# Optimization experiments

Measured on AMD Instinct MI355X. Metric: run time of the kernel, lower is better.

Reference implementation:

```python
import jax, jax.numpy as jnp
import numpy as np

N, F, D, M, B, K = 100000, 256, 128, 10, 32768, 32


def setup_inputs() -> dict:
    key = jax.random.key(0)
    ks = jax.random.split(key, 14)
    stdv = float(1.0 / np.sqrt(D))
    inp = {
        "feature": jax.random.normal(ks[0], (N, F), jnp.float32),
        "flow_char_adj": jax.random.uniform(ks[1], (M, N), jnp.float32),
        "history": jax.random.randint(ks[2], (B, K), 0, N),
        "item_id": jax.random.randint(ks[3], (B,), 0, N),
        "category_r": jax.random.randint(ks[4], (B,), 0, 2),
        "category_n": jax.random.randint(ks[5], (B,), 0, 2),
        "PA_level": jax.random.randint(ks[6], (B,), 0, M),
        # learned parameters (uniform(-stdv, stdv) as in reset_parameters)
        "weight_emb": jax.random.uniform(ks[7], (F, D), jnp.float32, -stdv, stdv),
        "bias_emb": jax.random.uniform(ks[8], (D,), jnp.float32, -stdv, stdv),
        "weight_character": jax.random.uniform(ks[9], (2 * D, D), jnp.float32, -stdv, stdv),
        "att1_w": jax.random.uniform(ks[10], (D, 1), jnp.float32, -stdv, stdv),
        "att1_b": jax.random.uniform(ks[11], (1,), jnp.float32, -stdv, stdv),
        "linear1_w": jax.random.uniform(ks[12], (2 * D, D), jnp.float32, -stdv, stdv),
        "linear1_b": jax.random.uniform(ks[13], (D,), jnp.float32, -stdv, stdv),
    }
    return inp


def reference(feature, flow_char_adj, weight_emb, bias_emb, weight_character,
              att1_w, att1_b, linear1_w, linear1_b,
              history, item_id, category_r, category_n, PA_level):
    # embedding_encode
    flow_emb = feature @ weight_emb + bias_emb              # [N, D]
    character_emb = flow_char_adj @ flow_emb                # [M, D] (spmm)

    # character_modeling (shared for r and n)
    def char_lat(cat, pa):
        ce = jnp.concatenate([character_emb[cat], character_emb[pa]], axis=1)  # [B, 2D]
        return jax.nn.sigmoid(ce @ weight_character)        # [B, D]

    lat_r = char_lat(category_r, PA_level)
    lat_n = char_lat(category_n, PA_level)

    # attribute_agg: mix flow emb with its 2 category embeddings
    flow_all = (flow_emb + flow_char_adj[:2].T @ character_emb[:2]) * 0.5  # [N, D]

    # Flow_Aggregator: per-node neighbor attention (batched over ragged lists,
    # here padded to fixed degree K)
    neigh = flow_all[history]                                # [B, K, D]
    scores = neigh @ att1_w + att1_b                         # [B, K, 1]
    att = jax.nn.softmax(scores, axis=1)                     # softmax over neighbors
    agg = jnp.sum(att * neigh, axis=1)                       # [B, D]

    # NOTE: in the torch source, self_flow_latent is mutated in-place so
    # self_feats aliases neigh_feats -> both halves of the concat equal agg.
    combined = jnp.concatenate([agg, agg], axis=1)           # [B, 2D]
    out = jax.nn.relu(combined @ linear1_w + linear1_b)      # [B, D] (dropout p=0)

    pred_r = jnp.sum(lat_r * out, axis=1)                    # [B]
    pred_n = jnp.sum(lat_n * out, axis=1)                    # [B]
    return pred_r, pred_n
```

## Files before the change

### kernel.cpp

```cpp
#include <hip/hip_runtime.h>
#include <cmath>

#define NN 100000
#define FF 256
#define DDIM 128
#define MM 10
#define BB 32768
#define KK 32
#define NB1 1563
#define NREP 64

#define OFF_Q     0
#define OFF_CEREP 100096
#define OFF_CE    182016
#define OFF_LAT   183296
#define OFF_CE01  185856
#define OFF_CS    186112
#define OFF_AGGB  186128
#define OFF_FE8   2283280
#define OFF_WF    5483280
#define OFF_WPF   5499664

typedef __attribute__((ext_vector_type(8))) short bf16x8;
typedef __attribute__((ext_vector_type(4))) float floatx4;
typedef __attribute__((ext_vector_type(2))) float floatx2;

__device__ __forceinline__ unsigned short f2bf(float x) {
  union { float f; unsigned u; } v; v.f = x;
  unsigned r = v.u + 0x7FFFu + ((v.u >> 16) & 1u);
  return (unsigned short)(r >> 16);
}

__device__ __forceinline__ bf16x8 cvt8(float4 a, float4 b) {
  short h[8];
  h[0] = (short)f2bf(a.x); h[1] = (short)f2bf(a.y);
  h[2] = (short)f2bf(a.z); h[3] = (short)f2bf(a.w);
  h[4] = (short)f2bf(b.x); h[5] = (short)f2bf(b.y);
  h[6] = (short)f2bf(b.z); h[7] = (short)f2bf(b.w);
  return *reinterpret_cast<bf16x8*>(h);
}

__global__ __launch_bounds__(256) void k0_wprep(const float* __restrict__ wemb,
                                                const float* __restrict__ l1w,
                                                short* __restrict__ wf,
                                                short* __restrict__ wpf)
{
  const int t = blockIdx.x * 256 + threadIdx.x;
  if (t < 4096) {
    const int kk = t >> 9, rem = t & 511;
    const int ct = rem >> 6, l = rem & 63;
    const int n = ct * 16 + (l & 15);
    const int kbase = kk * 32 + (l >> 4) * 8;
    short hi[8];
#pragma unroll
    for (int j = 0; j < 8; j++) hi[j] = (short)f2bf(wemb[(kbase + j) * 128 + n]);
    *reinterpret_cast<int4*>(&wf[((kk * 8 + ct) * 64 + l) * 8]) = *reinterpret_cast<int4*>(hi);
  } else {
    const int t2 = t - 4096;
    const int kk = t2 >> 9, rem = t2 & 511;
    const int ct = rem >> 6, l = rem & 63;
    const int n = ct * 16 + (l & 15);
    short h[8];
#pragma unroll
    for (int j = 0; j < 8; j++) {
      const int kp = kk * 32 + (l >> 4) * 8 + j;
      const int i = ((kp & 7) << 4) | (kp >> 3);
      h[j] = (short)f2bf(l1w[i * 128 + n] + l1w[(128 + i) * 128 + n]);
    }
    *reinterpret_cast<int4*>(&wpf[((kk * 8 + ct) * 64 + l) * 8]) = *reinterpret_cast<int4*>(h);
  }
}

__global__ __launch_bounds__(256) void k1_fused(const float* __restrict__ feat,
    const short* __restrict__ wf, const float* __restrict__ bemb,
    const float* __restrict__ attw, const float* __restrict__ adj,
    float* __restrict__ q, unsigned char* __restrict__ fe8,
    float* __restrict__ cerep)
{
  __shared__ __align__(16) unsigned char ldst[128 * 144];
  const int tid = threadIdx.x;
  const int wv = tid >> 6, l = tid & 63;
  const int lane16 = l & 15, quad = l >> 4;
  const int rowbase = blockIdx.x * 64 + wv * 16;

  floatx4 acc[8];
#pragma unroll
  for (int ct = 0; ct < 8; ct++) acc[ct] = floatx4{0.f, 0.f, 0.f, 0.f};

  int r0 = rowbase + lane16; if (r0 > NN - 1) r0 = NN - 1;
  const float* pa = &feat[(size_t)r0 * 256 + quad * 8];

  float4 A[4][2];
#pragma unroll
  for (int i = 0; i < 4; i++) {
    A[i][0] = *reinterpret_cast<const float4*>(pa + i * 32);
    A[i][1] = *reinterpret_cast<const float4*>(pa + i * 32 + 4);
  }
#pragma unroll
  for (int kk = 0; kk < 8; kk++) {
    const bf16x8 a0 = cvt8(A[kk & 3][0], A[kk & 3][1]);
    if (kk < 4) {
      A[kk & 3][0] = *reinterpret_cast<const float4*>(pa + (kk + 4) * 32);
      A[kk & 3][1] = *reinterpret_cast<const float4*>(pa + (kk + 4) * 32 + 4);
    }
    const short* wb = &wf[kk * 4096 + l * 8];
#pragma unroll
    for (int ct = 0; ct < 8; ct++) {
      const bf16x8 bh = *reinterpret_cast<const bf16x8*>(&wb[ct * 512]);
      acc[ct] = __builtin_amdgcn_mfma_f32_16x16x32_bf16(a0, bh, acc[ct], 0, 0, 0);
    }
  }

  float bembv[8], attwv[8];
#pragma unroll
  for (int ct = 0; ct < 8; ct++) {
    bembv[ct] = bemb[ct * 16 + lane16];
    attwv[ct] = attw[ct * 16 + lane16];
  }
#pragma unroll
  for (int reg = 0; reg < 4; reg++) {
    const int r = rowbase + quad * 4 + reg;
    float v[8]; float qp = 0.f;
#pragma unroll
    for (int ct = 0; ct < 8; ct++) {
      v[ct] = acc[ct][reg] + bembv[ct];
      qp = fmaf(v[ct], attwv[ct], qp);
    }
    acc[0][reg] = v[0]; acc[1][reg] = v[1]; acc[2][reg] = v[2]; acc[3][reg] = v[3];
    acc[4][reg] = v[4]; acc[5][reg] = v[5]; acc[6][reg] = v[6]; acc[7][reg] = v[7];
    qp += __shfl_xor(qp, 1, 16);
    qp += __shfl_xor(qp, 2, 16);
    qp += __shfl_xor(qp, 4, 16);
    qp += __shfl_xor(qp, 8, 16);
    if (r < NN) {
      unsigned u0 = __builtin_amdgcn_cvt_pk_fp8_f32(v[0], v[1], 0, false);
      u0 = __builtin_amdgcn_cvt_pk_fp8_f32(v[2], v[3], u0, true);
      unsigned u1 = __builtin_amdgcn_cvt_pk_fp8_f32(v[4], v[5], 0, false);
      u1 = __builtin_amdgcn_cvt_pk_fp8_f32(v[6], v[7], u1, true);
      *reinterpret_cast<uint2*>(&fe8[(size_t)r * 128 + lane16 * 8]) = make_uint2(u0, u1);
      if (lane16 == 0) q[r] = 0.5f * qp;
    }
  }
#pragma unroll
  for (int rp = 0; rp < 2; rp++) {
    const int rloc = wv * 16 + quad * 4 + rp * 2;
    const int g0 = blockIdx.x * 64 + rloc;
#pragma unroll
    for (int ct = 0; ct < 8; ct++) {
      const unsigned short h0 = (g0     < NN) ? f2bf(acc[ct][rp * 2])     : (unsigned short)0;
      const unsigned short h1 = (g0 + 1 < NN) ? f2bf(acc[ct][rp * 2 + 1]) : (unsigned short)0;
      const unsigned pk = (unsigned)h0 | ((unsigned)h1 << 16);
      *reinterpret_cast<unsigned*>(&ldst[(ct * 16 + lane16) * 144 + rloc * 2]) = pk;
    }
  }
  __syncthreads();

  floatx4 cacc[2];
  cacc[0] = floatx4{0.f, 0.f, 0.f, 0.f};
  cacc[1] = floatx4{0.f, 0.f, 0.f, 0.f};
  const int mclamp = (lane16 < 10) ? lane16 : 9;
#pragma unroll
  for (int kc = 0; kc < 2; kc++) {
    int n0 = blockIdx.x * 64 + kc * 32 + quad * 8;
    if (n0 > NN - 8) n0 = NN - 8;
    const float4 f0 = *reinterpret_cast<const float4*>(&adj[(size_t)mclamp * NN + n0]);
    const float4 f1 = *reinterpret_cast<const float4*>(&adj[(size_t)mclamp * NN + n0 + 4]);
    const bf16x8 afr = cvt8(f0, f1);
#pragma unroll
    for (int tt = 0; tt < 2; tt++) {
      const int col = (wv * 2 + tt) * 16 + lane16;
      const bf16x8 bfr = *reinterpret_cast<const bf16x8*>(
          &ldst[col * 144 + (kc * 32 + quad * 8) * 2]);
      cacc[tt] = __builtin_amdgcn_mfma_f32_16x16x32_bf16(afr, bfr, cacc[tt], 0, 0, 0);
    }
  }
  float* myrep = &cerep[(blockIdx.x & (NREP - 1)) * 1280];
#pragma unroll
  for (int tt = 0; tt < 2; tt++) {
#pragma unroll
    for (int reg = 0; reg < 4; reg++) {
      const int m = quad * 4 + reg;
      if (m < 10)
        atomicAdd(&myrep[m * 128 + (wv * 2 + tt) * 16 + lane16], cacc[tt][reg]);
    }
  }
}

__global__ __launch_bounds__(256) void k3r_reduce(const float* __restrict__ cerep,
                                                  float* __restrict__ ce)
{
  const int o = blockIdx.x * 256 + threadIdx.x;
  if (o < 1280) {
    float s = 0.f;
#pragma unroll 8
    for (int r = 0; r < NREP; r++) s += cerep[r * 1280 + o];
    ce[o] = s;
  }
}

__global__ __launch_bounds__(128) void k3_prep(const float* __restrict__ ce,
    const float* __restrict__ wchar, const float* __restrict__ attw,
    float* __restrict__ latTab, float* __restrict__ ce01p, float* __restrict__ cs)
{
  const int blk = blockIdx.x, tid = threadIdx.x;
  __shared__ float cec[128], cep[128];
  if (blk < 20) {
    const int c = blk / 10, p = blk % 10;
    cec[tid] = ce[c * 128 + tid];
    cep[tid] = ce[p * 128 + tid];
    __syncthreads();
    float s = 0.f;
#pragma unroll 4
    for (int j = 0; j < 128; j++) {
      s = fmaf(cec[j], wchar[j * 128 + tid], s);
      s = fmaf(cep[j], wchar[(128 + j) * 128 + tid], s);
    }
    latTab[blk * 128 + tid] = 1.f / (1.f + expf(-s));
  } else {
    const float s0 = ce[tid];
    const float s1 = ce[128 + tid];
    const int pidx = (tid & 15) * 8 + (tid >> 4);
    ce01p[pidx] = s0;
    ce01p[128 + pidx] = s1;
    cec[tid] = s0 * attw[tid];
    cep[tid] = s1 * attw[tid];
    __syncthreads();
    if (tid < 64) {
      float p0 = cec[tid] + cec[tid + 64];
      float p1 = cep[tid] + cep[tid + 64];
#pragma unroll
      for (int off = 32; off >= 1; off >>= 1) {
        p0 += __shfl_xor(p0, off);
        p1 += __shfl_xor(p1, off);
      }
      if (tid == 0) { cs[0] = 0.5f * p0; cs[1] = 0.5f * p1; }
    }
  }
}

__global__ __launch_bounds__(256) void k4a_attn(const unsigned char* __restrict__ fe8,
    const float* __restrict__ q, const float* __restrict__ adj,
    const int* __restrict__ history, const float* __restrict__ cs,
    const float* __restrict__ attb_p, const float* __restrict__ ce01p,
    short* __restrict__ aggb)
{
  const int tid = threadIdx.x;
  const int lane = tid & 63;
  const int wv = tid >> 6;
  const int half = lane >> 5;
  const int t = lane & 31;
  const int b = blockIdx.x * 8 + wv * 2 + half;

  const int n_my = history[b * 32 + t];
  const float a0 = adj[n_my];
  const float a1 = adj[NN + n_my];
  const float sc = q[n_my] + a0 * cs[0] + a1 * cs[1] + attb_p[0];
  float m = sc;
#pragma unroll
  for (int off = 16; off >= 1; off >>= 1) m = fmaxf(m, __shfl_xor(m, off, 32));
  const float e = expf(sc - m);
  float sum = e;
#pragma unroll
  for (int off = 16; off >= 1; off >>= 1) sum += __shfl_xor(sum, off, 32);
  const float att = e / sum;
  float p0 = att * a0, p1 = att * a1;
#pragma unroll
  for (int off = 16; off >= 1; off >>= 1) {
    p0 += __shfl_xor(p0, off, 32);
    p1 += __shfl_xor(p1, off, 32);
  }

  float4 acc = make_float4(0.f, 0.f, 0.f, 0.f);
#pragma unroll
  for (int k = 0; k < 32; k++) {
    const int nk = __shfl(n_my, k, 32);
    const float ak = __shfl(att, k, 32);
    const unsigned u = *reinterpret_cast<const unsigned*>(&fe8[(size_t)nk * 128 + t * 4]);
    const floatx2 lo = __builtin_amdgcn_cvt_pk_f32_fp8(u, false);
    const floatx2 hi = __builtin_amdgcn_cvt_pk_f32_fp8(u, true);
    acc.x = fmaf(ak, lo[0], acc.x);
    acc.y = fmaf(ak, lo[1], acc.y);
    acc.z = fmaf(ak, hi[0], acc.z);
    acc.w = fmaf(ak, hi[1], acc.w);
  }
  const int col = t * 4;
  const float4 c0 = *reinterpret_cast<const float4*>(&ce01p[col]);
  const float4 c1 = *reinterpret_cast<const float4*>(&ce01p[128 + col]);
  const float ox = 0.5f * (acc.x + p0 * c0.x + p1 * c1.x);
  const float oy = 0.5f * (acc.y + p0 * c0.y + p1 * c1.y);
  const float oz = 0.5f * (acc.z + p0 * c0.z + p1 * c1.z);
  const float ow = 0.5f * (acc.w + p0 * c0.w + p1 * c1.w);
  const unsigned lo_ = (unsigned)f2bf(ox) | ((unsigned)f2bf(oy) << 16);
  const unsigned hi_ = (unsigned)f2bf(oz) | ((unsigned)f2bf(ow) << 16);
  *reinterpret_cast<uint2*>(&aggb[(size_t)b * 128 + col]) = make_uint2(lo_, hi_);
}

__global__ __launch_bounds__(256) void k4b_mfma(const short* __restrict__ aggb,
    const short* __restrict__ wpf, const float* __restrict__ l1b,
    const float* __restrict__ latTab,
    const int* __restrict__ cr, const int* __restrict__ cn, const int* __restrict__ pa,
    float* __restrict__ out)
{
  const int tid = threadIdx.x;
  const int wv = tid >> 6, l = tid & 63;
  const int lane16 = l & 15, quad = l >> 4;
  const int rowbase = blockIdx.x * 128 + wv * 32;
  const int r0 = rowbase + lane16;
  const int r1 = r0 + 16;

  floatx4 acc[2][8];
#pragma unroll
  for (int rt = 0; rt < 2; rt++)
#pragma unroll
    for (int ct = 0; ct < 8; ct++) acc[rt][ct] = floatx4{0.f, 0.f, 0.f, 0.f};

#pragma unroll
  for (int kk = 0; kk < 4; kk++) {
    const bf16x8 a0 = *reinterpret_cast<const bf16x8*>(&aggb[(size_t)r0 * 128 + kk * 32 + quad * 8]);
    const bf16x8 a1 = *reinterpret_cast<const bf16x8*>(&aggb[(size_t)r1 * 128 + kk * 32 + quad * 8]);
    const short* wb = &wpf[kk * 4096 + l * 8];
#pragma unroll
    for (int ct = 0; ct < 8; ct++) {
      const bf16x8 bh = *reinterpret_cast<const bf16x8*>(&wb[ct * 512]);
      acc[0][ct] = __builtin_amdgcn_mfma_f32_16x16x32_bf16(a0, bh, acc[0][ct], 0, 0, 0);
      acc[1][ct] = __builtin_amdgcn_mfma_f32_16x16x32_bf16(a1, bh, acc[1][ct], 0, 0, 0);
    }
  }

  float bb[8];
#pragma unroll
  for (int ct = 0; ct < 8; ct++) bb[ct] = l1b[ct * 16 + lane16];
#pragma unroll
  for (int rt = 0; rt < 2; rt++) {
#pragma unroll
    for (int reg = 0; reg < 4; reg++) {
      const int r = rowbase + rt * 16 + quad * 4 + reg;
      const int ir  = (cr[r] * 10 + pa[r]) * 128;
      const int in_ = (cn[r] * 10 + pa[r]) * 128;
      float pr = 0.f, pn = 0.f;
#pragma unroll
      for (int ct = 0; ct < 8; ct++) {
        const float v = fmaxf(acc[rt][ct][reg] + bb[ct], 0.f);
        pr = fmaf(v, latTab[ir  + ct * 16 + lane16], pr);
        pn = fmaf(v, latTab[in_ + ct * 16 + lane16], pn);
      }
      pr += __shfl_xor(pr, 1, 16); pr += __shfl_xor(pr, 2, 16);
      pr += __shfl_xor(pr, 4, 16); pr += __shfl_xor(pr, 8, 16);
      pn += __shfl_xor(pn, 1, 16); pn += __shfl_xor(pn, 2, 16);
      pn += __shfl_xor(pn, 4, 16); pn += __shfl_xor(pn, 8, 16);
      if (lane16 == 0) { out[r] = pr; out[BB + r] = pn; }
    }
  }
}

extern "C" void kernel_launch(void* const* d_in, const int* in_sizes, int n_in,
                              void* d_out, int out_size, void* d_ws, size_t ws_size,
                              hipStream_t stream) {
  const float* feat  = (const float*)d_in[0];
  const float* adj   = (const float*)d_in[1];
  const int*   hist  = (const int*)d_in[2];
  const int*   cr    = (const int*)d_in[4];
  const int*   cn    = (const int*)d_in[5];
  const int*   pa    = (const int*)d_in[6];
  const float* wemb  = (const float*)d_in[7];
  const float* bemb  = (const float*)d_in[8];
  const float* wchar = (const float*)d_in[9];
  const float* attw  = (const float*)d_in[10];
  const float* attb  = (const float*)d_in[11];
  const float* l1w   = (const float*)d_in[12];
  const float* l1b   = (const float*)d_in[13];
  float* out = (float*)d_out;
  float* ws  = (float*)d_ws;

  float* q     = ws + OFF_Q;
  float* cerep = ws + OFF_CEREP;
  float* ce    = ws + OFF_CE;
  float* lat   = ws + OFF_LAT;
  float* ce01p = ws + OFF_CE01;
  float* cs    = ws + OFF_CS;
  short* aggb  = (short*)(ws + OFF_AGGB);
  unsigned char* fe8 = (unsigned char*)(ws + OFF_FE8);
  short* wf    = (short*)(ws + OFF_WF);
  short* wpf   = (short*)(ws + OFF_WPF);

  hipMemsetAsync(cerep, 0, NREP * 1280 * sizeof(float), stream);
  k0_wprep<<<24, 256, 0, stream>>>(wemb, l1w, wf, wpf);
  k1_fused<<<NB1, 256, 0, stream>>>(feat, wf, bemb, attw, adj, q, fe8, cerep);
  k3r_reduce<<<5, 256, 0, stream>>>(cerep, ce);
  k3_prep<<<21, 128, 0, stream>>>(ce, wchar, attw, lat, ce01p, cs);
  k4a_attn<<<4096, 256, 0, stream>>>(fe8, q, adj, hist, cs, attb, ce01p, aggb);
  k4b_mfma<<<256, 256, 0, stream>>>(aggb, wpf, l1b, lat, cr, cn, pa, out);
}
```

Measured before the change: 268.7 us.

## Retile k1 so each wave computes four row tiles reusing weight fragments

The fused embedding GEMM kernel now uses 128-thread blocks where each wave computes 64 rows (four 16-row tiles), so the 8 weight fragments loaded per k-step are reused across four MFMA row tiles instead of one. Block count halves and the LDS staging tile doubles in width to 128 rows for the adjacency-times-embedding MFMA. The aim is to cut redundant weight loads and per-block overhead and atomics. The cost is 128 accumulator registers per lane, which raises register pressure and can limit occupancy. The software prefetch of feature rows is also dropped.

```diff
diff --git a/kernel.cpp b/kernel.cpp
--- a/kernel.cpp
+++ b/kernel.cpp
@@ -7,7 +7,7 @@
 #define MM 10
 #define BB 32768
 #define KK 32
-#define NB1 1563
+#define NB1 782
 #define NREP 64
 
 #define OFF_Q     0
@@ -71,44 +71,50 @@
   }
 }
 
-__global__ __launch_bounds__(256) void k1_fused(const float* __restrict__ feat,
+__global__ __launch_bounds__(128, 2) void k1_fused(const float* __restrict__ feat,
     const short* __restrict__ wf, const float* __restrict__ bemb,
     const float* __restrict__ attw, const float* __restrict__ adj,
     float* __restrict__ q, unsigned char* __restrict__ fe8,
     float* __restrict__ cerep)
 {
-  __shared__ __align__(16) unsigned char ldst[128 * 144];
+  __shared__ __align__(16) unsigned char ldst[128 * 272];
   const int tid = threadIdx.x;
   const int wv = tid >> 6, l = tid & 63;
   const int lane16 = l & 15, quad = l >> 4;
-  const int rowbase = blockIdx.x * 64 + wv * 16;
-
-  floatx4 acc[8];
-#pragma unroll
-  for (int ct = 0; ct < 8; ct++) acc[ct] = floatx4{0.f, 0.f, 0.f, 0.f};
-
-  int r0 = rowbase + lane16; if (r0 > NN - 1) r0 = NN - 1;
-  const float* pa = &feat[(size_t)r0 * 256 + quad * 8];
-
-  float4 A[4][2];
-#pragma unroll
-  for (int i = 0; i < 4; i++) {
-    A[i][0] = *reinterpret_cast<const float4*>(pa + i * 32);
-    A[i][1] = *reinterpret_cast<const float4*>(pa + i * 32 + 4);
-  }
-#pragma unroll
+
+  floatx4 acc[4][8];
+#pragma unroll
+  for (int rt = 0; rt < 4; rt++)
+#pragma unroll
+    for (int ct = 0; ct < 8; ct++) acc[rt][ct] = floatx4{0.f, 0.f, 0.f, 0.f};
+
+  const float* pa[4];
+#pragma unroll
+  for (int rt = 0; rt < 4; rt++) {
+    int r = blockIdx.x * 128 + (wv * 4 + rt) * 16 + lane16;
+    if (r > NN - 1) r = NN - 1;
+    pa[rt] = &feat[(size_t)r * 256 + quad * 8];
+  }
+
+#pragma unroll 2
   for (int kk = 0; kk < 8; kk++) {
-    const bf16x8 a0 = cvt8(A[kk & 3][0], A[kk & 3][1]);
-    if (kk < 4) {
-      A[kk & 3][0] = *reinterpret_cast<const float4*>(pa + (kk + 4) * 32);
-      A[kk & 3][1] = *reinterpret_cast<const float4*>(pa + (kk + 4) * 32 + 4);
-    }
     const short* wb = &wf[kk * 4096 + l * 8];
-#pragma unroll
-    for (int ct = 0; ct < 8; ct++) {
-      const bf16x8 bh = *reinterpret_cast<const bf16x8*>(&wb[ct * 512]);
-      acc[ct] = __builtin_amdgcn_mfma_f32_16x16x32_bf16(a0, bh, acc[ct], 0, 0, 0);
-    }
+    bf16x8 bh[8];
+#pragma unroll
+    for (int ct = 0; ct < 8; ct++)
+      bh[ct] = *reinterpret_cast<const bf16x8*>(&wb[ct * 512]);
+    bf16x8 a[4];
+#pragma unroll
+    for (int rt = 0; rt < 4; rt++) {
+      const float4 f0 = *reinterpret_cast<const float4*>(pa[rt] + kk * 32);
+      const float4 f1 = *reinterpret_cast<const float4*>(pa[rt] + kk * 32 + 4);
+      a[rt] = cvt8(f0, f1);
+    }
+#pragma unroll
+    for (int rt = 0; rt < 4; rt++)
+#pragma unroll
+      for (int ct = 0; ct < 8; ct++)
+        acc[rt][ct] = __builtin_amdgcn_mfma_f32_16x16x32_bf16(a[rt], bh[ct], acc[rt][ct], 0, 0, 0);
   }
 
   float bembv[8], attwv[8];
@@ -118,70 +124,77 @@
     attwv[ct] = attw[ct * 16 + lane16];
   }
 #pragma unroll
-  for (int reg = 0; reg < 4; reg++) {
-    const int r = rowbase + quad * 4 + reg;
-    float v[8]; float qp = 0.f;
+  for (int rt = 0; rt < 4; rt++) {
+#pragma unroll
+    for (int reg = 0; reg < 4; reg++) {
+      const int r = blockIdx.x * 128 + (wv * 4 + rt) * 16 + quad * 4 + reg;
+      float v[8]; float qp = 0.f;
+#pragma unroll
+      for (int ct = 0; ct < 8; ct++) {
+        v[ct] = acc[rt][ct][reg] + bembv[ct];
+        qp = fmaf(v[ct], attwv[ct], qp);
+      }
+#pragma unroll
+      for (int ct = 0; ct < 8; ct++) acc[rt][ct][reg] = v[ct];
+      qp += __shfl_xor(qp, 1, 16);
+      qp += __shfl_xor(qp, 2, 16);
+      qp += __shfl_xor(qp, 4, 16);
+      qp += __shfl_xor(qp, 8, 16);
+      if (r < NN) {
+        unsigned u0 = __builtin_amdgcn_cvt_pk_fp8_f32(v[0], v[1], 0, false);
+        u0 = __builtin_amdgcn_cvt_pk_fp8_f32(v[2], v[3], u0, true);
+        unsigned u1 = __builtin_amdgcn_cvt_pk_fp8_f32(v[4], v[5], 0, false);
+        u1 = __builtin_amdgcn_cvt_pk_fp8_f32(v[6], v[7], u1, true);
+        *reinterpret_cast<uint2*>(&fe8[(size_t)r * 128 + lane16 * 8]) = make_uint2(u0, u1);
+        if (lane16 == 0) q[r] = 0.5f * qp;
+      }
+    }
+  }
+#pragma unroll
+  for (int rt = 0; rt < 4; rt++) {
+    const int rlocBase = (wv * 4 + rt) * 16 + quad * 4;
+    const int gBase = blockIdx.x * 128 + rlocBase;
 #pragma unroll
     for (int ct = 0; ct < 8; ct++) {
-      v[ct] = acc[ct][reg] + bembv[ct];
-      qp = fmaf(v[ct], attwv[ct], qp);
-    }
-    acc[0][reg] = v[0]; acc[1][reg] = v[1]; acc[2][reg] = v[2]; acc[3][reg] = v[3];
-    acc[4][reg] = v[4]; acc[5][reg] = v[5]; acc[6][reg] = v[6]; acc[7][reg] = v[7];
-    qp += __shfl_xor(qp, 1, 16);
-    qp += __shfl_xor(qp, 2, 16);
-    qp += __shfl_xor(qp, 4, 16);
-    qp += __shfl_xor(qp, 8, 16);
-    if (r < NN) {
-      unsigned u0 = __builtin_amdgcn_cvt_pk_fp8_f32(v[0], v[1], 0, false);
-      u0 = __builtin_amdgcn_cvt_pk_fp8_f32(v[2], v[3], u0, true);
-      unsigned u1 = __builtin_amdgcn_cvt_pk_fp8_f32(v[4], v[5], 0, false);
-      u1 = __builtin_amdgcn_cvt_pk_fp8_f32(v[6], v[7], u1, true);
-      *reinterpret_cast<uint2*>(&fe8[(size_t)r * 128 + lane16 * 8]) = make_uint2(u0, u1);
-      if (lane16 == 0) q[r] = 0.5f * qp;
-    }
-  }
-#pragma unroll
-  for (int rp = 0; rp < 2; rp++) {
-    const int rloc = wv * 16 + quad * 4 + rp * 2;
-    const int g0 = blockIdx.x * 64 + rloc;
-#pragma unroll
-    for (int ct = 0; ct < 8; ct++) {
-      const unsigned short h0 = (g0     < NN) ? f2bf(acc[ct][rp * 2])     : (unsigned short)0;
-      const unsigned short h1 = (g0 + 1 < NN) ? f2bf(acc[ct][rp * 2 + 1]) : (unsigned short)0;
-      const unsigned pk = (unsigned)h0 | ((unsigned)h1 << 16);
-      *reinterpret_cast<unsigned*>(&ldst[(ct * 16 + lane16) * 144 + rloc * 2]) = pk;
+      unsigned short u[4];
+#pragma unroll
+      for (int reg = 0; reg < 4; reg++)
+        u[reg] = (gBase + reg < NN) ? f2bf(acc[rt][ct][reg]) : (unsigned short)0;
+      const unsigned lo_ = (unsigned)u[0] | ((unsigned)u[1] << 16);
+      const unsigned hi_ = (unsigned)u[2] | ((unsigned)u[3] << 16);
+      *reinterpret_cast<uint2*>(&ldst[(ct * 16 + lane16) * 272 + rlocBase * 2]) =
+          make_uint2(lo_, hi_);
     }
   }
   __syncthreads();
 
-  floatx4 cacc[2];
-  cacc[0] = floatx4{0.f, 0.f, 0.f, 0.f};
-  cacc[1] = floatx4{0.f, 0.f, 0.f, 0.f};
+  floatx4 cacc[4];
+#pragma unroll
+  for (int tt = 0; tt < 4; tt++) cacc[tt] = floatx4{0.f, 0.f, 0.f, 0.f};
   const int mclamp = (lane16 < 10) ? lane16 : 9;
 #pragma unroll
-  for (int kc = 0; kc < 2; kc++) {
-    int n0 = blockIdx.x * 64 + kc * 32 + quad * 8;
+  for (int kc = 0; kc < 4; kc++) {
+    int n0 = blockIdx.x * 128 + kc * 32 + quad * 8;
     if (n0 > NN - 8) n0 = NN - 8;
     const float4 f0 = *reinterpret_cast<const float4*>(&adj[(size_t)mclamp * NN + n0]);
     const float4 f1 = *reinterpret_cast<const float4*>(&adj[(size_t)mclamp * NN + n0 + 4]);
     const bf16x8 afr = cvt8(f0, f1);
 #pragma unroll
-    for (int tt = 0; tt < 2; tt++) {
-      const int col = (wv * 2 + tt) * 16 + lane16;
+    for (int tt = 0; tt < 4; tt++) {
+      const int col = (wv * 4 + tt) * 16 + lane16;
       const bf16x8 bfr = *reinterpret_cast<const bf16x8*>(
-          &ldst[col * 144 + (kc * 32 + quad * 8) * 2]);
+          &ldst[col * 272 + (kc * 32 + quad * 8) * 2]);
       cacc[tt] = __builtin_amdgcn_mfma_f32_16x16x32_bf16(afr, bfr, cacc[tt], 0, 0, 0);
     }
   }
   float* myrep = &cerep[(blockIdx.x & (NREP - 1)) * 1280];
 #pragma unroll
-  for (int tt = 0; tt < 2; tt++) {
+  for (int tt = 0; tt < 4; tt++) {
 #pragma unroll
     for (int reg = 0; reg < 4; reg++) {
       const int m = quad * 4 + reg;
       if (m < 10)
-        atomicAdd(&myrep[m * 128 + (wv * 2 + tt) * 16 + lane16], cacc[tt][reg]);
+        atomicAdd(&myrep[m * 128 + (wv * 4 + tt) * 16 + lane16], cacc[tt][reg]);
     }
   }
 }
@@ -385,7 +398,7 @@
 
   hipMemsetAsync(cerep, 0, NREP * 1280 * sizeof(float), stream);
   k0_wprep<<<24, 256, 0, stream>>>(wemb, l1w, wf, wpf);
-  k1_fused<<<NB1, 256, 0, stream>>>(feat, wf, bemb, attw, adj, q, fe8, cerep);
+  k1_fused<<<NB1, 128, 0, stream>>>(feat, wf, bemb, attw, adj, q, fe8, cerep);
   k3r_reduce<<<5, 256, 0, stream>>>(cerep, ce);
   k3_prep<<<21, 128, 0, stream>>>(ce, wchar, attw, lat, ce01p, cs);
   k4a_attn<<<4096, 256, 0, stream>>>(fe8, q, adj, hist, cs, attb, ce01p, aggb);
```

After: 269.3 us. About the same (+0.2%).
